# Performance work log

Measured on AMD Instinct MI355X. Metric: run time of the kernel, lower is better.

The kernel has to match this reference:

```python
import jax, jax.numpy as jnp
import numpy as np

N_NODES = 50000
N_EDGES = 800000
IN_DIM = 128
HIDDEN = 256
N_CLASSES = 16
N_GRAPHS = 128


def setup_inputs() -> dict:
    key = jax.random.key(0)
    ks = jax.random.split(key, 10)
    x = jax.random.normal(ks[0], (N_NODES, IN_DIM), dtype=jnp.float32)
    edge_index = jax.random.randint(ks[1], (2, N_EDGES), 0, N_NODES, dtype=jnp.int64)
    batch = jnp.sort(jax.random.randint(ks[2], (N_NODES,), 0, N_GRAPHS, dtype=jnp.int64))
    s = 1.0 / np.sqrt(HIDDEN)
    return {
        "x": x,
        "edge_index": edge_index,
        "batch": batch,
        "W_in": jax.random.normal(ks[3], (IN_DIM, HIDDEN), dtype=jnp.float32) / np.sqrt(IN_DIM),
        "b_in": jnp.zeros((HIDDEN,), dtype=jnp.float32),
        "W1": jax.random.normal(ks[4], (HIDDEN, HIDDEN), dtype=jnp.float32) * s,
        "b1": jnp.zeros((HIDDEN,), dtype=jnp.float32),
        "W2": jax.random.normal(ks[5], (HIDDEN, HIDDEN), dtype=jnp.float32) * s,
        "b2": jnp.zeros((HIDDEN,), dtype=jnp.float32),
        "W_out": jax.random.normal(ks[6], (HIDDEN, N_CLASSES), dtype=jnp.float32) * s,
        "b_out": jnp.zeros((N_CLASSES,), dtype=jnp.float32),
    }


def gcn_conv(x, W, b, src, dst):
    # PyG GCNConv: add self-loops, symmetric norm D^-1/2 A D^-1/2, scatter-add at target.
    h = x @ W  # [N, H]
    n = x.shape[0]
    # degree of target nodes, including one self-loop per node
    deg = jax.ops.segment_sum(jnp.ones_like(dst, dtype=h.dtype), dst, num_segments=n) + 1.0
    dinv = deg ** -0.5  # [N]
    norm = dinv[src] * dinv[dst]  # [E]
    msg = h[src] * norm[:, None]  # [E, H]  gather + scale
    agg = jax.ops.segment_sum(msg, dst, num_segments=n)  # scatter-add
    agg = agg + h * (dinv * dinv)[:, None]  # self-loop contribution
    return agg + b


def reference(x, edge_index, batch, W_in, b_in, W1, b1, W2, b2, W_out, b_out):
    src, dst = edge_index[0], edge_index[1]
    h = x @ W_in + b_in
    # layer 1 (dropout is identity in eval mode)
    h = jax.nn.relu(gcn_conv(h, W1, b1, src, dst))
    # layer 2
    h = jax.nn.relu(gcn_conv(h, W2, b2, src, dst))
    # global mean pool over graphs
    sums = jax.ops.segment_sum(h, batch, num_segments=N_GRAPHS)  # [G, H]
    counts = jax.ops.segment_sum(jnp.ones((h.shape[0],), h.dtype), batch, num_segments=N_GRAPHS)
    pooled = sums / jnp.maximum(counts, 1.0)[:, None]
    return pooled @ W_out + b_out  # [G, n_classes]
```

## Files before the change

kernel.cpp:

```cpp
#include <hip/hip_runtime.h>
#include <hip/hip_bf16.h>

typedef __attribute__((ext_vector_type(8))) short bf16x8;
typedef __attribute__((ext_vector_type(4))) float f32x4;

__device__ __forceinline__ unsigned short f2bf(float f) {
    unsigned u = __float_as_uint(f);
    u += 0x7fff + ((u >> 16) & 1);
    return (unsigned short)(u >> 16);
}
__device__ __forceinline__ float bf2f(unsigned short s) {
    return __uint_as_float(((unsigned)s) << 16);
}

#define GL2LDS16(g, l) __builtin_amdgcn_global_load_lds(                      \
        (const __attribute__((address_space(1))) void*)(g),                   \
        (__attribute__((address_space(3))) void*)(l), 16, 0, 0)


__global__ __launch_bounds__(256) void fused_misc_kernel(
        const int* __restrict__ dst, int* __restrict__ cnt, int e,
        const float* __restrict__ W2, unsigned short* __restrict__ Wt2,
        const float* __restrict__ x, unsigned short* __restrict__ xb, int n4,
        const float* __restrict__ W_in, const float* __restrict__ b_in,
        const float* __restrict__ W1,
        unsigned short* __restrict__ WfT, float* __restrict__ bv,
        int CB, int TB, int XB) {
    __shared__ float row[256];
    int b = blockIdx.x;
    if (b < CB) {
        int i = b * 256 + threadIdx.x;
        if (i < e) atomicAdd(&cnt[dst[i]], 1);
    } else if (b < CB + TB) {
        int i = (b - CB) * 256 + threadIdx.x;
        int k = i >> 8, nn = i & 255;
        Wt2[(size_t)nn * 256 + k] = f2bf(W2[i]);
    } else if (b < CB + TB + XB) {
        int i = (b - CB - TB) * 256 + threadIdx.x;
        if (i < n4) {
            float4 v = ((const float4*)x)[i];
            ushort4 o;
            o.x = f2bf(v.x); o.y = f2bf(v.y); o.z = f2bf(v.z); o.w = f2bf(v.w);
            ((ushort4*)xb)[i] = o;
        }
    } else {
        int k = b - (CB + TB + XB);
        int nn = threadIdx.x;
        row[nn] = (k < 128) ? W_in[k * 256 + nn] : b_in[nn];
        __syncthreads();
        float acc = 0.f;
        #pragma unroll 4
        for (int j = 0; j < 256; ++j) acc = fmaf(row[j], W1[j * 256 + nn], acc);
        if (k < 128) WfT[(size_t)nn * 128 + k] = f2bf(acc);
        else bv[nn] = acc;
    }
}


__global__ __launch_bounds__(256) void fill_kernel(const int* __restrict__ src,
                                                   const int* __restrict__ dst,
                                                   int* __restrict__ cursor,
                                                   unsigned short* __restrict__ csr16,
                                                   const int* __restrict__ deg,
                                                   float* __restrict__ dinv,
                                                   int e, int n, int FB) {
    int b = blockIdx.x;
    if (b < FB) {
        int i = b * 256 + threadIdx.x;
        if (i < e) {
            int d = dst[i];
            int p = atomicAdd(&cursor[d], 1);
            if (p < 64) csr16[((size_t)d << 6) + p] = (unsigned short)src[i];
        }
    } else {
        int i = (b - FB) * 256 + threadIdx.x;
        if (i < n) dinv[i] = rsqrtf((float)deg[i] + 1.0f);
    }
}


template <int MODE>
__global__ __launch_bounds__(256) void gemm_bf16(const unsigned short* __restrict__ A,
                                                 const unsigned short* __restrict__ Wt,
                                                 const float* __restrict__ aux,
                                                 const float* __restrict__ aux2,
                                                 const float* __restrict__ aux3,
                                                 unsigned short* __restrict__ C,
                                                 int M, int K) {
    __shared__ unsigned short As[128 * 64];
    __shared__ unsigned short Bs[128 * 64];
    const int tid  = threadIdx.x;
    const int lane = tid & 63;
    const int w    = tid >> 6;
    const int wr   = w >> 1, wc = w & 1;
    const int row0 = blockIdx.x * 128;
    const int col0 = blockIdx.y * 128;
    const int mlane = lane & 15, quad = lane >> 4;

    f32x4 acc[4][4];
    #pragma unroll
    for (int i = 0; i < 4; ++i)
        #pragma unroll
        for (int j = 0; j < 4; ++j) acc[i][j] = f32x4{0.f, 0.f, 0.f, 0.f};

    const unsigned short* gA[4]; const unsigned short* gB[4];
    unsigned short* lA[4]; unsigned short* lB[4];
    #pragma unroll
    for (int p = 0; p < 4; ++p) {
        int cid = (p * 4 + w) * 64 + lane;
        int row = cid >> 3, slot = cid & 7;
        int rowA = row0 + row; if (rowA >= M) rowA = M - 1;
        gA[p] = A + (size_t)rowA * K + slot * 8;
        gB[p] = Wt + (size_t)(col0 + row) * K + slot * 8;
        lA[p] = &As[((p * 4 + w) * 64) * 8];
        lB[p] = &Bs[((p * 4 + w) * 64) * 8];
    }

    for (int k0 = 0; k0 < K; k0 += 64) {
        #pragma unroll
        for (int p = 0; p < 4; ++p) GL2LDS16(gA[p] + k0, lA[p]);
        #pragma unroll
        for (int p = 0; p < 4; ++p) GL2LDS16(gB[p] + k0, lB[p]);
        __syncthreads();
        #pragma unroll
        for (int ks = 0; ks < 2; ++ks) {
            bf16x8 af[4], bfv[4];
            #pragma unroll
            for (int i = 0; i < 4; ++i)
                af[i] = *(const bf16x8*)&As[(wr * 64 + i * 16 + mlane) * 64 + ks * 32 + quad * 8];
            #pragma unroll
            for (int j = 0; j < 4; ++j)
                bfv[j] = *(const bf16x8*)&Bs[(wc * 64 + j * 16 + mlane) * 64 + ks * 32 + quad * 8];
            #pragma unroll
            for (int i = 0; i < 4; ++i)
                #pragma unroll
                for (int j = 0; j < 4; ++j)
                    acc[i][j] = __builtin_amdgcn_mfma_f32_16x16x32_bf16(af[i], bfv[j], acc[i][j], 0, 0, 0);
        }
        __syncthreads();
    }

    float bj[4], cj[4];
    if (MODE == 0) {
        #pragma unroll
        for (int j = 0; j < 4; ++j) bj[j] = aux[col0 + wc * 64 + j * 16 + mlane];
    } else if (MODE == 2) {
        #pragma unroll
        for (int j = 0; j < 4; ++j) {
            int gcol = col0 + wc * 64 + j * 16 + mlane;
            bj[j] = aux2[gcol];
            cj[j] = aux3[gcol];
        }
    }
    #pragma unroll
    for (int i = 0; i < 4; ++i) {
        #pragma unroll
        for (int r = 0; r < 4; ++r) {
            int grow = row0 + wr * 64 + i * 16 + quad * 4 + r;
            if (grow < M) {
                float d = (MODE != 0) ? aux[grow] : 0.f;
                #pragma unroll
                for (int j = 0; j < 4; ++j) {
                    int gcol = col0 + wc * 64 + j * 16 + mlane;
                    float v = acc[i][j][r];
                    if (MODE == 0)      v = v + bj[j];
                    else if (MODE == 1) v = v * d;
                    else {              v = fmaf(d, bj[j], v) + cj[j]; v = fmaxf(v, 0.f); }
                    C[(size_t)grow * 256 + gcol] = f2bf(v);
                }
            }
        }
    }
}


__global__ __launch_bounds__(256) void agg_x_kernel(const unsigned short* __restrict__ xb,
                                                    const int* __restrict__ deg,
                                                    const unsigned short* __restrict__ csr16,
                                                    const float* __restrict__ dinv,
                                                    unsigned short* __restrict__ ax,
                                                    float* __restrict__ s_out, int n) {
    int node = blockIdx.x * 4 + (threadIdx.x >> 6);
    if (node >= n) return;
    int lane = threadIdx.x & 63;
    int half = lane >> 5, hl = lane & 31;
    const ushort4* x4 = (const ushort4*)xb;
    int cnt = deg[node]; if (cnt > 64) cnt = 64;
    size_t beg = (size_t)node << 6;
    float dn = dinv[node];
    float a0 = 0.f, a1 = 0.f, a2 = 0.f, a3 = 0.f;
    float sdl = 0.f;

    int myi = 0; float mydv = 0.f;
    if (lane < cnt) { myi = (int)csr16[beg + lane]; mydv = dinv[myi]; sdl += mydv; }
    int j = 0;
    for (; j + 8 <= cnt; j += 8) {
        int s0 = __shfl(myi, j + half),     s1 = __shfl(myi, j + 2 + half);
        int s2 = __shfl(myi, j + 4 + half), s3 = __shfl(myi, j + 6 + half);
        float d0 = __shfl(mydv, j + half),     d1 = __shfl(mydv, j + 2 + half);
        float d2 = __shfl(mydv, j + 4 + half), d3 = __shfl(mydv, j + 6 + half);
        ushort4 v0 = x4[(size_t)s0 * 32 + hl];
        ushort4 v1 = x4[(size_t)s1 * 32 + hl];
        ushort4 v2 = x4[(size_t)s2 * 32 + hl];
        ushort4 v3 = x4[(size_t)s3 * 32 + hl];
        a0 = fmaf(bf2f(v0.x), d0, a0); a1 = fmaf(bf2f(v0.y), d0, a1);
        a2 = fmaf(bf2f(v0.z), d0, a2); a3 = fmaf(bf2f(v0.w), d0, a3);
        a0 = fmaf(bf2f(v1.x), d1, a0); a1 = fmaf(bf2f(v1.y), d1, a1);
        a2 = fmaf(bf2f(v1.z), d1, a2); a3 = fmaf(bf2f(v1.w), d1, a3);
        a0 = fmaf(bf2f(v2.x), d2, a0); a1 = fmaf(bf2f(v2.y), d2, a1);
        a2 = fmaf(bf2f(v2.z), d2, a2); a3 = fmaf(bf2f(v2.w), d2, a3);
        a0 = fmaf(bf2f(v3.x), d3, a0); a1 = fmaf(bf2f(v3.y), d3, a1);
        a2 = fmaf(bf2f(v3.z), d3, a2); a3 = fmaf(bf2f(v3.w), d3, a3);
    }
    for (; j < cnt; j += 2) {
        int jj = j + half; int sel = (jj < cnt) ? jj : j;
        int s_ = __shfl(myi, sel);
        float dd = __shfl(mydv, sel);
        if (jj >= cnt) dd = 0.f;
        ushort4 v = x4[(size_t)s_ * 32 + hl];
        a0 = fmaf(bf2f(v.x), dd, a0); a1 = fmaf(bf2f(v.y), dd, a1);
        a2 = fmaf(bf2f(v.z), dd, a2); a3 = fmaf(bf2f(v.w), dd, a3);
    }

    a0 += __shfl_xor(a0, 32); a1 += __shfl_xor(a1, 32);
    a2 += __shfl_xor(a2, 32); a3 += __shfl_xor(a3, 32);
    float sd = sdl;
    #pragma unroll
    for (int off = 32; off > 0; off >>= 1) sd += __shfl_down(sd, off);
    if (lane < 32) {
        ushort4 sv = x4[(size_t)node * 32 + hl];
        a0 = fmaf(dn, bf2f(sv.x), a0) * dn;
        a1 = fmaf(dn, bf2f(sv.y), a1) * dn;
        a2 = fmaf(dn, bf2f(sv.z), a2) * dn;
        a3 = fmaf(dn, bf2f(sv.w), a3) * dn;
        ushort4 r;
        r.x = f2bf(a0); r.y = f2bf(a1); r.z = f2bf(a2); r.w = f2bf(a3);
        ((ushort4*)ax)[(size_t)node * 32 + hl] = r;
        if (lane == 0) s_out[node] = dn * (sd + dn);
    }
}


__global__ __launch_bounds__(256) void agg_kernel(const unsigned short* __restrict__ hs,
                                                  const int* __restrict__ deg,
                                                  const unsigned short* __restrict__ csr16,
                                                  const float* __restrict__ dinv,
                                                  const float* __restrict__ bias,
                                                  unsigned short* __restrict__ out, int n) {
    int node = blockIdx.x * 4 + (threadIdx.x >> 6);
    if (node >= n) return;
    int lane = threadIdx.x & 63;
    const ushort4* hs4 = (const ushort4*)hs;
    int cnt = deg[node]; if (cnt > 64) cnt = 64;
    size_t beg = (size_t)node << 6;
    ushort4 sv = hs4[(size_t)node * 64 + lane];
    float a0 = bf2f(sv.x), a1 = bf2f(sv.y), a2 = bf2f(sv.z), a3 = bf2f(sv.w);
    float c0 = 0.f, c1 = 0.f, c2 = 0.f, c3 = 0.f;

    int myi = (lane < cnt) ? (int)csr16[beg + lane] : 0;
    int j = 0;
    for (; j + 8 <= cnt; j += 8) {
        int s0 = __shfl(myi, j + 0), s1 = __shfl(myi, j + 1);
        int s2 = __shfl(myi, j + 2), s3 = __shfl(myi, j + 3);
        int s4 = __shfl(myi, j + 4), s5 = __shfl(myi, j + 5);
        int s6 = __shfl(myi, j + 6), s7 = __shfl(myi, j + 7);
        ushort4 v0 = hs4[(size_t)s0 * 64 + lane];
        ushort4 v1 = hs4[(size_t)s1 * 64 + lane];
        ushort4 v2 = hs4[(size_t)s2 * 64 + lane];
        ushort4 v3 = hs4[(size_t)s3 * 64 + lane];
        ushort4 v4 = hs4[(size_t)s4 * 64 + lane];
        ushort4 v5 = hs4[(size_t)s5 * 64 + lane];
        ushort4 v6 = hs4[(size_t)s6 * 64 + lane];
        ushort4 v7 = hs4[(size_t)s7 * 64 + lane];
        a0 += bf2f(v0.x) + bf2f(v1.x) + bf2f(v2.x) + bf2f(v3.x);
        a1 += bf2f(v0.y) + bf2f(v1.y) + bf2f(v2.y) + bf2f(v3.y);
        a2 += bf2f(v0.z) + bf2f(v1.z) + bf2f(v2.z) + bf2f(v3.z);
        a3 += bf2f(v0.w) + bf2f(v1.w) + bf2f(v2.w) + bf2f(v3.w);
        c0 += bf2f(v4.x) + bf2f(v5.x) + bf2f(v6.x) + bf2f(v7.x);
        c1 += bf2f(v4.y) + bf2f(v5.y) + bf2f(v6.y) + bf2f(v7.y);
        c2 += bf2f(v4.z) + bf2f(v5.z) + bf2f(v6.z) + bf2f(v7.z);
        c3 += bf2f(v4.w) + bf2f(v5.w) + bf2f(v6.w) + bf2f(v7.w);
    }
    for (; j < cnt; ++j) {
        int s = __shfl(myi, j);
        ushort4 v = hs4[(size_t)s * 64 + lane];
        a0 += bf2f(v.x); a1 += bf2f(v.y); a2 += bf2f(v.z); a3 += bf2f(v.w);
    }
    a0 += c0; a1 += c1; a2 += c2; a3 += c3;

    float d = dinv[node];
    float4 b = ((const float4*)bias)[lane];
    ushort4 r;
    r.x = f2bf(fmaxf(fmaf(a0, d, b.x), 0.f));
    r.y = f2bf(fmaxf(fmaf(a1, d, b.y), 0.f));
    r.z = f2bf(fmaxf(fmaf(a2, d, b.z), 0.f));
    r.w = f2bf(fmaxf(fmaf(a3, d, b.w), 0.f));
    ((ushort4*)out)[(size_t)node * 64 + lane] = r;
}


__global__ __launch_bounds__(256) void pool_partial_kernel(const unsigned short* __restrict__ h,
                                                           const int* __restrict__ batch,
                                                           float* __restrict__ sums,
                                                           int* __restrict__ counts,
                                                           int n, int chunk) {
    int beg = blockIdx.x * chunk;
    int end = beg + chunk; if (end > n) end = n;
    if (beg >= end) return;
    int c = threadIdx.x;
    int curg = batch[beg];
    float acc = 0.f;
    int runlen = 0;
    for (int i = beg; i < end; ++i) {
        int g = batch[i];
        if (g != curg) {
            atomicAdd(&sums[(size_t)curg * 256 + c], acc);
            if (c == 0) atomicAdd(&counts[curg], runlen);
            acc = 0.f; runlen = 0; curg = g;
        }
        acc += bf2f(h[(size_t)i * 256 + c]);
        ++runlen;
    }
    atomicAdd(&sums[(size_t)curg * 256 + c], acc);
    if (c == 0) atomicAdd(&counts[curg], runlen);
}

__global__ __launch_bounds__(256) void pool_final_kernel(const float* __restrict__ sums,
                                                         const int* __restrict__ counts,
                                                         const float* __restrict__ Wout,
                                                         const float* __restrict__ bout,
                                                         float* __restrict__ out) {
    __shared__ float pl[256];
    int g = blockIdx.x;
    int c = threadIdx.x;
    int cnt = counts[g];
    pl[c] = sums[(size_t)g * 256 + c] / (float)(cnt > 0 ? cnt : 1);
    __syncthreads();
    if (c < 16) {
        float o = bout[c];
        #pragma unroll 4
        for (int k = 0; k < 256; ++k) o = fmaf(pl[k], Wout[k * 16 + c], o);
        out[g * 16 + c] = o;
    }
}


extern "C" void kernel_launch(void* const* d_in, const int* in_sizes, int n_in,
                              void* d_out, int out_size, void* d_ws, size_t ws_size,
                              hipStream_t stream) {
    const float* x     = (const float*)d_in[0];
    const int*   ei    = (const int*)d_in[1];
    const int*   batch = (const int*)d_in[2];
    const float* W_in  = (const float*)d_in[3];
    const float* b_in  = (const float*)d_in[4];
    const float* W1    = (const float*)d_in[5];
    const float* b1    = (const float*)d_in[6];
    const float* W2    = (const float*)d_in[7];
    const float* b2    = (const float*)d_in[8];
    const float* Wout  = (const float*)d_in[9];
    const float* bout  = (const float*)d_in[10];

    const int E = in_sizes[1] / 2;
    const int N = in_sizes[2];
    const int IN_DIM = in_sizes[0] / N;
    const int G = 128;
    const int* src = ei;
    const int* dst = ei + E;

    char* ws = (char*)d_ws;
    size_t off = 0;
    auto alloc = [&](size_t bytes) { size_t p = off; off += (bytes + 255) & ~(size_t)255; return p; };
    unsigned short* bufA = (unsigned short*)(ws + alloc((size_t)N * 256 * 2));
    unsigned short* bufB = (unsigned short*)(ws + alloc((size_t)N * 256 * 2));
    unsigned short* xb   = (unsigned short*)(ws + alloc((size_t)N * IN_DIM * 2));
    unsigned short* Wt2  = (unsigned short*)(ws + alloc((size_t)256 * 256 * 2));
    unsigned short* WfT  = (unsigned short*)(ws + alloc((size_t)256 * IN_DIM * 2));
    float*          bv   = (float*)(ws + alloc((size_t)256 * 4));
    float*          sbuf = (float*)(ws + alloc((size_t)N * 4));
    size_t zbeg = off;
    int*   deg_cnt = (int*)(ws + alloc((size_t)N * 4));
    float* sums    = (float*)(ws + alloc((size_t)G * 256 * 4));
    int*   counts  = (int*)(ws + alloc((size_t)G * 4));
    int*   cursor  = (int*)(ws + alloc((size_t)N * 4));
    size_t zend = off;
    float* dinv    = (float*)(ws + alloc((size_t)N * 4));
    unsigned short* csr16 = (unsigned short*)(ws + alloc((size_t)N * 64 * 2));
    (void)ws_size;

    unsigned short* axb = bufB;

    const int NB  = (N + 255) / 256;
    const int CB  = (E + 255) / 256;
    const int TB  = (256 * 256 + 255) / 256;
    const int XB  = (N * IN_DIM / 4 + 255) / 256;
    const int WB  = 129;
    const int FB  = (E + 255) / 256;

    hipMemsetAsync(ws + zbeg, 0, zend - zbeg, stream);
    fused_misc_kernel<<<CB + TB + XB + WB, 256, 0, stream>>>(
        dst, deg_cnt, E, W2, Wt2, x, xb, N * IN_DIM / 4,
        W_in, b_in, W1, WfT, bv, CB, TB, XB);
    fill_kernel<<<FB + NB, 256, 0, stream>>>(src, dst, cursor, csr16, deg_cnt, dinv, E, N, FB);

    agg_x_kernel<<<(N + 3) / 4, 256, 0, stream>>>(xb, deg_cnt, csr16, dinv, axb, sbuf, N);
    dim3 gg((N + 127) / 128, 2);
    gemm_bf16<2><<<gg, 256, 0, stream>>>(axb, WfT, sbuf, bv, b1, bufA, N, IN_DIM);

    gemm_bf16<1><<<gg, 256, 0, stream>>>(bufA, Wt2, dinv, nullptr, nullptr, bufB, N, 256);
    agg_kernel<<<(N + 3) / 4, 256, 0, stream>>>(bufB, deg_cnt, csr16, dinv, b2, bufA, N);

    const int PBLOCKS = 512;
    int chunk = (N + PBLOCKS - 1) / PBLOCKS;
    pool_partial_kernel<<<PBLOCKS, 256, 0, stream>>>(bufA, batch, sums, counts, N, chunk);
    pool_final_kernel<<<G, 256, 0, stream>>>(sums, counts, Wout, bout, (float*)d_out);
}
```

Measured before the change: 367.8 us.

## Reuse fill cursor as degree count and transpose W2 via shared tiles

Drops the separate atomic degree-count pass over all edges and uses the final fill cursor values as in-degrees, so the edge atomics run once instead of twice. The W2 bf16 transpose now goes through a padded shared-memory tile so both the reads and the writes are coalesced. The fused preprocessing kernel shrinks, and dinv becomes its own small kernel that must run after fill, which adds one launch and serialises the dinv computation after the edge pass.

```diff
diff --git a/kernel.cpp b/kernel.cpp
--- a/kernel.cpp
+++ b/kernel.cpp
@@ -19,32 +19,17 @@
 
 
 __global__ __launch_bounds__(256) void fused_misc_kernel(
-        const int* __restrict__ dst, int* __restrict__ cnt, int e,
         const float* __restrict__ W2, unsigned short* __restrict__ Wt2,
         const float* __restrict__ x, unsigned short* __restrict__ xb, int n4,
         const float* __restrict__ W_in, const float* __restrict__ b_in,
         const float* __restrict__ W1,
         unsigned short* __restrict__ WfT, float* __restrict__ bv,
-        int CB, int TB, int XB) {
+        int WB) {
     __shared__ float row[256];
+    __shared__ unsigned short tile[64][65];
     int b = blockIdx.x;
-    if (b < CB) {
-        int i = b * 256 + threadIdx.x;
-        if (i < e) atomicAdd(&cnt[dst[i]], 1);
-    } else if (b < CB + TB) {
-        int i = (b - CB) * 256 + threadIdx.x;
-        int k = i >> 8, nn = i & 255;
-        Wt2[(size_t)nn * 256 + k] = f2bf(W2[i]);
-    } else if (b < CB + TB + XB) {
-        int i = (b - CB - TB) * 256 + threadIdx.x;
-        if (i < n4) {
-            float4 v = ((const float4*)x)[i];
-            ushort4 o;
-            o.x = f2bf(v.x); o.y = f2bf(v.y); o.z = f2bf(v.z); o.w = f2bf(v.w);
-            ((ushort4*)xb)[i] = o;
-        }
-    } else {
-        int k = b - (CB + TB + XB);
+    if (b < WB) {
+        int k = b;
         int nn = threadIdx.x;
         row[nn] = (k < 128) ? W_in[k * 256 + nn] : b_in[nn];
         __syncthreads();
@@ -53,29 +38,58 @@
         for (int j = 0; j < 256; ++j) acc = fmaf(row[j], W1[j * 256 + nn], acc);
         if (k < 128) WfT[(size_t)nn * 128 + k] = f2bf(acc);
         else bv[nn] = acc;
-    }
-}
-
-
-__global__ __launch_bounds__(256) void fill_kernel(const int* __restrict__ src,
-                                                   const int* __restrict__ dst,
-                                                   int* __restrict__ cursor,
-                                                   unsigned short* __restrict__ csr16,
-                                                   const int* __restrict__ deg,
-                                                   float* __restrict__ dinv,
-                                                   int e, int n, int FB) {
-    int b = blockIdx.x;
-    if (b < FB) {
-        int i = b * 256 + threadIdx.x;
-        if (i < e) {
-            int d = dst[i];
-            int p = atomicAdd(&cursor[d], 1);
-            if (p < 64) csr16[((size_t)d << 6) + p] = (unsigned short)src[i];
+    } else if (b < WB + 16) {
+        int t = b - WB;
+        int ti = t >> 2, tj = t & 3;
+        int rq = threadIdx.x >> 4;
+        int c0 = (threadIdx.x & 15) * 4;
+        #pragma unroll
+        for (int rr = 0; rr < 64; rr += 16) {
+            int r = rr + rq;
+            float4 v = *(const float4*)&W2[(size_t)(ti * 64 + r) * 256 + tj * 64 + c0];
+            tile[r][c0]     = f2bf(v.x);
+            tile[r][c0 + 1] = f2bf(v.y);
+            tile[r][c0 + 2] = f2bf(v.z);
+            tile[r][c0 + 3] = f2bf(v.w);
+        }
+        __syncthreads();
+        #pragma unroll
+        for (int rr = 0; rr < 64; rr += 16) {
+            int nrow = rr + rq;
+            ushort4 o;
+            o.x = tile[c0][nrow];
+            o.y = tile[c0 + 1][nrow];
+            o.z = tile[c0 + 2][nrow];
+            o.w = tile[c0 + 3][nrow];
+            *(ushort4*)&Wt2[(size_t)(tj * 64 + nrow) * 256 + ti * 64 + c0] = o;
         }
     } else {
-        int i = (b - FB) * 256 + threadIdx.x;
-        if (i < n) dinv[i] = rsqrtf((float)deg[i] + 1.0f);
-    }
+        int i = (b - WB - 16) * 256 + threadIdx.x;
+        if (i < n4) {
+            float4 v = ((const float4*)x)[i];
+            ushort4 o;
+            o.x = f2bf(v.x); o.y = f2bf(v.y); o.z = f2bf(v.z); o.w = f2bf(v.w);
+            ((ushort4*)xb)[i] = o;
+        }
+    }
+}
+
+
+__global__ void fill_kernel(const int* __restrict__ src, const int* __restrict__ dst,
+                            int* __restrict__ cursor, unsigned short* __restrict__ csr16,
+                            int e) {
+    int i = blockIdx.x * blockDim.x + threadIdx.x;
+    if (i < e) {
+        int d = dst[i];
+        int p = atomicAdd(&cursor[d], 1);
+        if (p < 64) csr16[((size_t)d << 6) + p] = (unsigned short)src[i];
+    }
+}
+
+__global__ __launch_bounds__(256) void dinv_kernel(const int* __restrict__ deg,
+                                                   float* __restrict__ dinv, int n) {
+    int i = blockIdx.x * 256 + threadIdx.x;
+    if (i < n) dinv[i] = rsqrtf((float)deg[i] + 1.0f);
 }
 
 
@@ -378,7 +392,6 @@
     float*          bv   = (float*)(ws + alloc((size_t)256 * 4));
     float*          sbuf = (float*)(ws + alloc((size_t)N * 4));
     size_t zbeg = off;
-    int*   deg_cnt = (int*)(ws + alloc((size_t)N * 4));
     float* sums    = (float*)(ws + alloc((size_t)G * 256 * 4));
     int*   counts  = (int*)(ws + alloc((size_t)G * 4));
     int*   cursor  = (int*)(ws + alloc((size_t)N * 4));
@@ -390,24 +403,22 @@
     unsigned short* axb = bufB;
 
     const int NB  = (N + 255) / 256;
-    const int CB  = (E + 255) / 256;
-    const int TB  = (256 * 256 + 255) / 256;
     const int XB  = (N * IN_DIM / 4 + 255) / 256;
     const int WB  = 129;
     const int FB  = (E + 255) / 256;
 
     hipMemsetAsync(ws + zbeg, 0, zend - zbeg, stream);
-    fused_misc_kernel<<<CB + TB + XB + WB, 256, 0, stream>>>(
-        dst, deg_cnt, E, W2, Wt2, x, xb, N * IN_DIM / 4,
-        W_in, b_in, W1, WfT, bv, CB, TB, XB);
-    fill_kernel<<<FB + NB, 256, 0, stream>>>(src, dst, cursor, csr16, deg_cnt, dinv, E, N, FB);
-
-    agg_x_kernel<<<(N + 3) / 4, 256, 0, stream>>>(xb, deg_cnt, csr16, dinv, axb, sbuf, N);
+    fused_misc_kernel<<<WB + 16 + XB, 256, 0, stream>>>(
+        W2, Wt2, x, xb, N * IN_DIM / 4, W_in, b_in, W1, WfT, bv, WB);
+    fill_kernel<<<FB, 256, 0, stream>>>(src, dst, cursor, csr16, E);
+    dinv_kernel<<<NB, 256, 0, stream>>>(cursor, dinv, N);
+
+    agg_x_kernel<<<(N + 3) / 4, 256, 0, stream>>>(xb, cursor, csr16, dinv, axb, sbuf, N);
     dim3 gg((N + 127) / 128, 2);
     gemm_bf16<2><<<gg, 256, 0, stream>>>(axb, WfT, sbuf, bv, b1, bufA, N, IN_DIM);
 
     gemm_bf16<1><<<gg, 256, 0, stream>>>(bufA, Wt2, dinv, nullptr, nullptr, bufB, N, 256);
-    agg_kernel<<<(N + 3) / 4, 256, 0, stream>>>(bufB, deg_cnt, csr16, dinv, b2, bufA, N);
+    agg_kernel<<<(N + 3) / 4, 256, 0, stream>>>(bufB, cursor, csr16, dinv, b2, bufA, N);
 
     const int PBLOCKS = 512;
     int chunk = (N + PBLOCKS - 1) / PBLOCKS;
```

Measured after the change: 338.2 us. 8.1% less time.
